# Optimization experiments

Hardware: AMD Instinct MI355X
Metric: run time of the kernel (lower is better)

Reference implementation:

```python
import jax, jax.numpy as jnp
import numpy as np

L, B, D = 1024, 4, 1024
E, K, H = 8, 2, 4096


def setup_inputs() -> dict:
    key = jax.random.key(0)
    ks = jax.random.split(key, 12)
    s_g = 1.0 / np.sqrt(D)
    s_h = 1.0 / np.sqrt(H)
    return {
        "inputs": jax.random.normal(ks[0], (L, B, D), jnp.float32),
        "task_param": jax.random.normal(ks[1], (B, D), jnp.float32),
        "gate_img_w": jax.random.normal(ks[2], (D, E), jnp.float32) * s_g,
        "gate_img_b": jnp.zeros((E,), jnp.float32),
        "gate_txt_w": jax.random.normal(ks[3], (D, E), jnp.float32) * s_g,
        "gate_txt_b": jnp.zeros((E,), jnp.float32),
        "task_gate_w": jax.random.normal(ks[4], (D, E), jnp.float32) * s_g,
        "task_gate_b": jnp.zeros((E,), jnp.float32),
        "alpha": jnp.float32(0.5),
        "w1": jax.random.normal(ks[5], (E, D, H), jnp.float32) * s_g,
        "w2": jax.random.normal(ks[6], (E, H, D), jnp.float32) * s_h,
        "is_text": 1,
    }


def reference(inputs, task_param, gate_img_w, gate_img_b, gate_txt_w, gate_txt_b,
              task_gate_w, task_gate_b, alpha, w1, w2, is_text):
    # task gate: (B, E) -> broadcast over L
    task_logits = (task_param @ task_gate_w + task_gate_b)[None]  # (1, B, E)
    if is_text:
        input_logits = inputs @ gate_txt_w + gate_txt_b  # (L, B, E)
    else:
        input_logits = inputs @ gate_img_w + gate_img_b
    gate_logits = (1.0 - alpha) * input_logits + alpha * task_logits  # (L, B, E)

    topk_vals, sel = jax.lax.top_k(gate_logits, K)  # (L, B, K)

    # auxiliary load-balancing loss
    soft = jax.nn.softmax(gate_logits.astype(jnp.float32), axis=-1)
    avg_weight = soft.mean(axis=(0, 1))                       # (E,)
    expert_mask = jax.nn.one_hot(sel, E).sum(axis=2)          # (L, B, E)
    avg_count = expert_mask.mean(axis=(0, 1))                 # (E,)
    l_aux = jnp.mean(avg_weight * avg_count) * E

    # renormalized top-k weights, combined per expert: (L, B, E)
    weights = jax.nn.softmax(topk_vals.astype(jnp.float32), axis=-1).astype(inputs.dtype)
    comb = jnp.sum(jax.nn.one_hot(sel, E, dtype=weights.dtype) * weights[..., None], axis=2)

    # dense per-expert FFN, weighted combine (loop over fixed small E)
    results = jnp.zeros_like(inputs)
    for e in range(E):
        h = jax.nn.gelu(inputs @ w1[e])      # (L, B, H)
        out = h @ w2[e]                      # (L, B, D)
        results = results + comb[..., e:e + 1] * out
    return results, l_aux.astype(jnp.float32)
```

## Files before the change

kernel.cpp:

```cpp
#include <hip/hip_runtime.h>
#include <hip/hip_bf16.h>
#include <math.h>

#define L_ 1024
#define B_ 4
#define D_ 1024
#define E_ 8
#define K_ 2
#define H_ 4096
#define T_ (L_*B_)
#define P_ (T_*K_)
#define PPAD (P_+256)

typedef unsigned short u16;
typedef __attribute__((ext_vector_type(4))) float f32x4;
typedef __attribute__((ext_vector_type(8))) short s16x8;

__device__ __forceinline__ u16 f2bf(float f) {
  uint32_t u = __float_as_uint(f);
  uint32_t r = (u + 0x7FFFu + ((u >> 16) & 1u)) >> 16;
  return (u16)r;
}
__device__ __forceinline__ float bf2f(u16 v) {
  return __uint_as_float((uint32_t)v << 16);
}
__device__ __forceinline__ float gelu_fast(float v) {
  float u = v * (1.0f + 0.044715f * v * v);
  float t = __expf(-1.5957691216057308f * u);
  return v / (1.0f + t);
}


__device__ void conv_block(const float* __restrict__ src, u16* __restrict__ dst,
                           int R, int C, int r0, int c0) {
  __shared__ float tile[64][65];
  int t = threadIdx.x;
  int tr = t >> 4, tc = (t & 15) * 4;
#pragma unroll
  for (int p = 0; p < 4; ++p) {
    int r = tr + p * 16;
    float4 v = *(const float4*)(src + (size_t)(r0 + r) * C + c0 + tc);
    tile[r][tc] = v.x; tile[r][tc+1] = v.y; tile[r][tc+2] = v.z; tile[r][tc+3] = v.w;
  }
  __syncthreads();
#pragma unroll
  for (int p = 0; p < 4; ++p) {
    int c = tr + p * 16;
    ushort4 o;
    o.x = f2bf(tile[tc+0][c]); o.y = f2bf(tile[tc+1][c]);
    o.z = f2bf(tile[tc+2][c]); o.w = f2bf(tile[tc+3][c]);
    *(ushort4*)(dst + (size_t)(c0 + c) * R + r0 + tc) = o;
  }
}

__global__ void prep(const float* __restrict__ w1, u16* __restrict__ w1b,
                     const float* __restrict__ x, const float* __restrict__ task_param,
                     const float* __restrict__ gw_img, const float* __restrict__ gb_img,
                     const float* __restrict__ gw_txt, const float* __restrict__ gb_txt,
                     const float* __restrict__ tgw, const float* __restrict__ tgb,
                     const float* __restrict__ alpha_p, const int* __restrict__ is_text_p,
                     float4* __restrict__ sel_w, float* __restrict__ prob_part,
                     int* __restrict__ count_part) {
  int gid = blockIdx.x;
  if (gid < 8192) {
    int gx = gid & 63, gy = (gid >> 6) & 15, e = gid >> 10;
    conv_block(w1 + (size_t)e * D_ * H_, w1b + (size_t)e * D_ * H_,
               D_, H_, gy * 64, gx * 64);
    return;
  }
  int bid = gid - 8192;
  __shared__ float wprob[4][8];
  __shared__ int wcnt[4][8];
  int wid = threadIdx.x >> 6, lane = threadIdx.x & 63;
  int t = bid * 4 + wid;
  int b = t & (B_ - 1);
  int it = is_text_p[0];
  const float* gw = it ? gw_txt : gw_img;
  const float* gb = it ? gb_txt : gb_img;
  float alpha = alpha_p[0];
  const float* xr = x + (size_t)t * D_;
  const float* tp = task_param + (size_t)b * D_;
  float acc[8] = {0,0,0,0,0,0,0,0};
  float tac[8] = {0,0,0,0,0,0,0,0};
  for (int i = 0; i < D_/64; ++i) {
    int d = i * 64 + lane;
    float xv = xr[d], tv = tp[d];
#pragma unroll
    for (int e = 0; e < 8; ++e) {
      acc[e] += xv * gw[d*8 + e];
      tac[e] += tv * tgw[d*8 + e];
    }
  }
#pragma unroll
  for (int e = 0; e < 8; ++e) {
#pragma unroll
    for (int off = 32; off > 0; off >>= 1) {
      acc[e] += __shfl_xor(acc[e], off);
      tac[e] += __shfl_xor(tac[e], off);
    }
  }
  float lg[8];
#pragma unroll
  for (int e = 0; e < 8; ++e)
    lg[e] = (1.0f - alpha) * (acc[e] + gb[e]) + alpha * (tac[e] + tgb[e]);
  float m = lg[0];
#pragma unroll
  for (int e = 1; e < 8; ++e) m = fmaxf(m, lg[e]);
  float pr[8], ps = 0.f;
#pragma unroll
  for (int e = 0; e < 8; ++e) { pr[e] = expf(lg[e] - m); ps += pr[e]; }
  float inv = 1.0f / ps;
  int i0 = 0; float v0 = lg[0];
#pragma unroll
  for (int e = 1; e < 8; ++e) if (lg[e] > v0) { v0 = lg[e]; i0 = e; }
  int i1 = -1; float v1 = -1e30f;
#pragma unroll
  for (int e = 0; e < 8; ++e) if (e != i0 && lg[e] > v1) { v1 = lg[e]; i1 = e; }
  float ex = expf(v1 - v0);
  float w0 = 1.0f / (1.0f + ex), w1v = ex / (1.0f + ex);
  if (lane == 0) {
    sel_w[t] = make_float4(__int_as_float(i0), __int_as_float(i1), w0, w1v);
#pragma unroll
    for (int e = 0; e < 8; ++e) {
      wprob[wid][e] = pr[e] * inv;
      wcnt[wid][e] = (i0 == e) + (i1 == e);
    }
  }
  __syncthreads();
  if (threadIdx.x < 8) {
    int e = threadIdx.x;
    prob_part[bid * 8 + e] = wprob[0][e] + wprob[1][e] + wprob[2][e] + wprob[3][e];
    count_part[bid * 8 + e] = wcnt[0][e] + wcnt[1][e] + wcnt[2][e] + wcnt[3][e];
  }
}

__global__ void finalize(const float* __restrict__ prob_part, const int* __restrict__ count_part,
                         int* __restrict__ meta, float* __restrict__ laux_out) {
  __shared__ float ps_[256];
  __shared__ int cs_[256];
  int t = threadIdx.x;
  int e = t & 7, s = t >> 3;
  float p = 0.f; int c = 0;
  for (int b = s; b < 1024; b += 32) { p += prob_part[b*8 + e]; c += count_part[b*8 + e]; }
  ps_[t] = p; cs_[t] = c;
  __syncthreads();
  for (int st = 16; st > 0; st >>= 1) {
    if (s < st) { ps_[t] += ps_[t + st*8]; cs_[t] += cs_[t + st*8]; }
    __syncthreads();
  }
  if (t == 0) {
    int off = 0; float laux = 0.f;
    int u1 = 0, u2 = 0;
    for (int ee = 0; ee < 8; ++ee) {
      int cnt = cs_[ee];
      meta[ee] = cnt;
      meta[8 + ee] = off;
      meta[16 + ee] = off;
      int nb = (cnt + 255) >> 8;
      meta[24 + ee] = nb;
      meta[32 + ee] = u1;
      meta[41 + ee] = u2;
      u1 += 16 * nb;
      u2 += 16 * nb;
      off += cnt;
      laux += (ps_[ee] * (1.0f/4096.0f)) * ((float)cnt * (1.0f/4096.0f));
    }
    meta[32 + 8] = u1;
    meta[41 + 8] = u2;
    meta[50] = 0;
    meta[51] = 0;
    *laux_out = laux;
  }
}

__global__ void scatter_gather(const float* __restrict__ x, const float4* __restrict__ sel_w,
                               int* __restrict__ cursors, float* __restrict__ pair_w,
                               int* __restrict__ pair_idx, u16* __restrict__ Xg) {
  int wid = threadIdx.x >> 6, lane = threadIdx.x & 63;
  int t = blockIdx.x * 4 + wid;
  float4 sw = sel_w[t];
  int s0 = __float_as_int(sw.x), s1 = __float_as_int(sw.y);
  int p0 = 0, p1 = 0;
  if (lane == 0) {
    p0 = atomicAdd(&cursors[s0], 1);
    p1 = atomicAdd(&cursors[s1], 1);
  }
  p0 = __shfl(p0, 0); p1 = __shfl(p1, 0);
  if (lane == 0) {
    pair_w[p0] = sw.z; pair_w[p1] = sw.w;
    pair_idx[t*2] = p0; pair_idx[t*2+1] = p1;
  }
  const float* xr = x + (size_t)t * D_;
  u16* d0 = Xg + (size_t)p0 * D_;
  u16* d1 = Xg + (size_t)p1 * D_;
#pragma unroll
  for (int i = 0; i < 4; ++i) {
    int c = i * 256 + lane * 4;
    float4 v = *(const float4*)(xr + c);
    ushort4 o;
    o.x = f2bf(v.x); o.y = f2bf(v.y); o.z = f2bf(v.z); o.w = f2bf(v.w);
    *(ushort4*)(d0 + c) = o;
    *(ushort4*)(d1 + c) = o;
  }
}

template<int EPI, int KDIM, int KLEN, int NOUT, int NPANEL, int KSPLIT, bool DOCONV>
__global__ __launch_bounds__(512, 2)
void gemm256(const u16* __restrict__ Tok, const u16* __restrict__ Wt,
             int* __restrict__ meta, const float* __restrict__ pair_w,
             u16* __restrict__ Hout, u16* __restrict__ Cout,
             const float* __restrict__ w2f, u16* __restrict__ w2b) {
  const int* offs = meta + 8;
  const int* nbx  = meta + 24;
  const int* ub   = (EPI == 0) ? meta + 32 : meta + 41;
  int* tick       = meta + ((EPI == 0) ? 50 : 51);

  __shared__ u16 As[2][16384];
  __shared__ u16 Bs[2][16384];
  __shared__ int s_u;
  int t = threadIdx.x, lane = t & 63, wid = t >> 6;
  int wf = wid & 1, wt = wid >> 1;

  int goff[4]; int ldso[4];
#pragma unroll
  for (int i = 0; i < 4; ++i) {
    int slot = i * 512 + t;
    int row = slot >> 3;
    int kk = (slot & 7) ^ (row & 7);
    goff[i] = row * KDIM + kk * 8;
    ldso[i] = slot * 8;
  }

  int aoff[8][2], boff[4][2];
#pragma unroll
  for (int r = 0; r < 8; ++r) {
    int row = wf * 128 + r * 16 + (lane & 15);
#pragma unroll
    for (int h = 0; h < 2; ++h) {
      int kk = h * 4 + (lane >> 4);
      aoff[r][h] = (row * 8 + (kk ^ (row & 7))) * 8;
    }
  }
#pragma unroll
  for (int f = 0; f < 4; ++f) {
    int row = wt * 64 + f * 16 + (lane & 15);
#pragma unroll
    for (int h = 0; h < 2; ++h) {
      int kk = h * 4 + (lane >> 4);
      boff[f][h] = (row * 8 + (kk ^ (row & 7))) * 8;
    }
  }

  constexpr int NT = KLEN / 64;
  int lr = lane & 15, lg4 = (lane >> 4) * 4;
  int Ugemm = ub[8];
  int Utot = DOCONV ? (Ugemm + 4096) : Ugemm;

  for (;;) {
    if (t == 0) s_u = atomicAdd(tick, 1);
    __syncthreads();
    int u = s_u;
    if (u >= Utot) break;

    if (DOCONV && u >= Ugemm) {
      int cu = u - Ugemm;
      int e = cu >> 9;
      int loc = cu & 511;
      int rb = loc >> 4, cb = loc & 15;
      int r0 = rb * 128, c0 = cb * 64;
      const float* src = w2f + (size_t)e * H_ * D_;
      u16* dst = w2b + (size_t)e * H_ * D_;
      float* tile = (float*)&As[0][0];
#pragma unroll
      for (int p = 0; p < 4; ++p) {
        int idx = p * 512 + t;
        int r = idx >> 4;
        int cq = (idx & 15) * 4;
        float4 v = *(const float4*)(src + (size_t)(r0 + r) * D_ + c0 + cq);
        float* tr = tile + r * 67 + cq;
        tr[0] = v.x; tr[1] = v.y; tr[2] = v.z; tr[3] = v.w;
      }
      __syncthreads();
      int c = t >> 3, rq0 = (t & 7) * 16;
#pragma unroll
      for (int j = 0; j < 16; j += 4) {
        ushort4 o;
        o.x = f2bf(tile[(rq0 + j + 0) * 67 + c]);
        o.y = f2bf(tile[(rq0 + j + 1) * 67 + c]);
        o.z = f2bf(tile[(rq0 + j + 2) * 67 + c]);
        o.w = f2bf(tile[(rq0 + j + 3) * 67 + c]);
        *(ushort4*)(dst + (size_t)(c0 + c) * H_ + r0 + rq0 + j) = o;
      }
      continue;
    }

    int e = 0;
    while (u >= ub[e + 1]) ++e;
    int ul = u - ub[e];
    int nb = nbx[e];
    int panel = ul / (nb * KSPLIT);
    int rem   = ul - panel * (nb * KSPLIT);
    int bx    = rem / KSPLIT;
    int ks    = rem - bx * KSPLIT;
    int ne  = meta[e];
    int off = offs[e];
    int kbase = ks * KLEN;
    u16* Cpart = Cout + (size_t)ks * P_ * D_;
    const u16* Wg = Wt + (size_t)e * NOUT * KDIM + (size_t)panel * 256 * KDIM + kbase;
    const u16* Tg = Tok + (size_t)(off + bx * 256) * KDIM + kbase;

    f32x4 acc[8][4] = {};
#pragma unroll
    for (int i = 0; i < 4; ++i) {
      __builtin_amdgcn_global_load_lds(
          (const __attribute__((address_space(1))) void*)(Wg + goff[i]),
          (__attribute__((address_space(3))) void*)(&As[0][ldso[i]]), 16, 0, 0);
      __builtin_amdgcn_global_load_lds(
          (const __attribute__((address_space(1))) void*)(Tg + goff[i]),
          (__attribute__((address_space(3))) void*)(&Bs[0][ldso[i]]), 16, 0, 0);
    }
    __syncthreads();
    int cur = 0;
    for (int tt = 0; tt < NT; ++tt) {
      if (tt + 1 < NT) {
        int k0 = (tt + 1) * 64;
        int nbuf = cur ^ 1;
#pragma unroll
        for (int i = 0; i < 4; ++i) {
          __builtin_amdgcn_global_load_lds(
              (const __attribute__((address_space(1))) void*)(Wg + goff[i] + k0),
              (__attribute__((address_space(3))) void*)(&As[nbuf][ldso[i]]), 16, 0, 0);
          __builtin_amdgcn_global_load_lds(
              (const __attribute__((address_space(1))) void*)(Tg + goff[i] + k0),
              (__attribute__((address_space(3))) void*)(&Bs[nbuf][ldso[i]]), 16, 0, 0);
        }
      }
      const u16* Ab = &As[cur][0]; const u16* Bb = &Bs[cur][0];
#pragma unroll
      for (int h = 0; h < 2; ++h) {
        s16x8 a[8], b[4];
#pragma unroll
        for (int r = 0; r < 8; ++r) a[r] = *(const s16x8*)(Ab + aoff[r][h]);
#pragma unroll
        for (int f = 0; f < 4; ++f) b[f] = *(const s16x8*)(Bb + boff[f][h]);
#pragma unroll
        for (int r = 0; r < 8; ++r)
#pragma unroll
          for (int f = 0; f < 4; ++f)
            acc[r][f] = __builtin_amdgcn_mfma_f32_16x16x32_bf16(a[r], b[f], acc[r][f], 0, 0, 0);
      }
      __syncthreads();
      cur ^= 1;
    }

#pragma unroll
    for (int f = 0; f < 4; ++f) {
      int tokl = bx * 256 + wt * 64 + f * 16 + lr;
      if (tokl >= ne) continue;
      size_t grow = (size_t)(off + tokl);
      if (EPI == 0) {
#pragma unroll
        for (int r = 0; r < 8; ++r) {
          ushort4 o;
          o.x = f2bf(gelu_fast(acc[r][f][0]));
          o.y = f2bf(gelu_fast(acc[r][f][1]));
          o.z = f2bf(gelu_fast(acc[r][f][2]));
          o.w = f2bf(gelu_fast(acc[r][f][3]));
          *(ushort4*)(Hout + grow * NOUT + panel * 256 + wf * 128 + r * 16 + lg4) = o;
        }
      } else {
        float w = pair_w[grow];
#pragma unroll
        for (int r = 0; r < 8; ++r) {
          ushort4 o;
          o.x = f2bf(acc[r][f][0] * w); o.y = f2bf(acc[r][f][1] * w);
          o.z = f2bf(acc[r][f][2] * w); o.w = f2bf(acc[r][f][3] * w);
          *(ushort4*)(Cpart + grow * NOUT + panel * 256 + wf * 128 + r * 16 + lg4) = o;
        }
      }
    }
  }
}

__global__ void combine(const u16* __restrict__ pair_out, const int* __restrict__ pair_idx,
                        float* __restrict__ out) {
  int t = blockIdx.x;
  int p0 = pair_idx[t*2], p1 = pair_idx[t*2+1];
  int c = threadIdx.x * 4;
  float ox = 0.f, oy = 0.f, oz = 0.f, ow = 0.f;
#pragma unroll
  for (int part = 0; part < 4; ++part) {
    const u16* pp = pair_out + (size_t)part * P_ * D_;
    ushort4 a = *(const ushort4*)(pp + (size_t)p0 * D_ + c);
    ushort4 b = *(const ushort4*)(pp + (size_t)p1 * D_ + c);
    ox += bf2f(a.x) + bf2f(b.x);
    oy += bf2f(a.y) + bf2f(b.y);
    oz += bf2f(a.z) + bf2f(b.z);
    ow += bf2f(a.w) + bf2f(b.w);
  }
  float4 o; o.x = ox; o.y = oy; o.z = oz; o.w = ow;
  *(float4*)(out + (size_t)t * D_ + c) = o;
}

extern "C" void kernel_launch(void* const* d_in, const int* in_sizes, int n_in,
                              void* d_out, int out_size, void* d_ws, size_t ws_size,
                              hipStream_t stream) {
  const float* inputs      = (const float*)d_in[0];
  const float* task_param  = (const float*)d_in[1];
  const float* gate_img_w  = (const float*)d_in[2];
  const float* gate_img_b  = (const float*)d_in[3];
  const float* gate_txt_w  = (const float*)d_in[4];
  const float* gate_txt_b  = (const float*)d_in[5];
  const float* task_gate_w = (const float*)d_in[6];
  const float* task_gate_b = (const float*)d_in[7];
  const float* alpha       = (const float*)d_in[8];
  const float* w1          = (const float*)d_in[9];
  const float* w2          = (const float*)d_in[10];
  const int*   is_text     = (const int*)d_in[11];
  float* out = (float*)d_out;

  char* ws = (char*)d_ws;
  u16* w1b = (u16*)(ws + 0);
  u16* w2b = (u16*)(ws + 67108864);
  u16* Xg  = (u16*)(ws + 134217728);
  u16* Hb  = (u16*)(ws + 151519232);
  float4* sel_w   = (float4*)(ws + 220725248);
  float* pair_w   = (float*)(ws + 220725248 + 65536);
  int* pair_idx   = (int*)(ws + 220725248 + 98816);
  float* prob_part= (float*)(ws + 220725248 + 131584);
  int* count_part = (int*)(ws + 220725248 + 164352);
  int* meta       = (int*)(ws + 220725248 + 197120);
  u16* pair_out   = (u16*)(ws + 0);

  prep<<<dim3(9216), 256, 0, stream>>>(w1, w1b,
      inputs, task_param, gate_img_w, gate_img_b, gate_txt_w, gate_txt_b,
      task_gate_w, task_gate_b, alpha, is_text, sel_w, prob_part, count_part);
  finalize<<<dim3(1), 256, 0, stream>>>(prob_part, count_part, meta,
      out + (size_t)T_ * D_);
  scatter_gather<<<dim3(T_/4), 256, 0, stream>>>(inputs, sel_w, meta + 16, pair_w, pair_idx, Xg);
  gemm256<0, D_, D_, H_, 16, 1, true><<<dim3(256), 512, 0, stream>>>(
      Xg, w1b, meta, pair_w, Hb, (u16*)nullptr, w2, w2b);
  gemm256<1, H_, H_/4, D_, 4, 4, false><<<dim3(256), 512, 0, stream>>>(
      Hb, w2b, meta, pair_w, (u16*)nullptr, pair_out, (const float*)nullptr, (u16*)nullptr);
  combine<<<dim3(T_), 256, 0, stream>>>(pair_out, pair_idx, out);
}
```

Baseline: 450.2 us.

## Shrink persistent grouped GEMM tiles to 128x128 with K=32 steps and more blocks

Rewrites the persistent grouped expert GEMM from 256x256 tiles with 512 threads and K-step 64 to 128x128 tiles with 256 threads, K-step 32 and a single 32KB shared buffer. The launch grows to 768 persistent blocks, and the in-GEMM w2 conversion now uses smaller 64x64 tiles through a shared helper. The aim is better occupancy and less tail and padding waste on small per-expert token counts. The cost is lower data reuse per tile, more tiles to schedule and twice as many barrier-separated K iterations.

```diff
diff --git a/kernel.cpp b/kernel.cpp
--- a/kernel.cpp
+++ b/kernel.cpp
@@ -31,24 +31,24 @@
 }
 
 
-__device__ void conv_block(const float* __restrict__ src, u16* __restrict__ dst,
-                           int R, int C, int r0, int c0) {
-  __shared__ float tile[64][65];
+__device__ void conv_tile(const float* __restrict__ src, u16* __restrict__ dst,
+                          int R, int C, int r0, int c0, float* tile ) {
   int t = threadIdx.x;
   int tr = t >> 4, tc = (t & 15) * 4;
 #pragma unroll
   for (int p = 0; p < 4; ++p) {
     int r = tr + p * 16;
     float4 v = *(const float4*)(src + (size_t)(r0 + r) * C + c0 + tc);
-    tile[r][tc] = v.x; tile[r][tc+1] = v.y; tile[r][tc+2] = v.z; tile[r][tc+3] = v.w;
+    float* tp = tile + r * 65 + tc;
+    tp[0] = v.x; tp[1] = v.y; tp[2] = v.z; tp[3] = v.w;
   }
   __syncthreads();
 #pragma unroll
   for (int p = 0; p < 4; ++p) {
     int c = tr + p * 16;
     ushort4 o;
-    o.x = f2bf(tile[tc+0][c]); o.y = f2bf(tile[tc+1][c]);
-    o.z = f2bf(tile[tc+2][c]); o.w = f2bf(tile[tc+3][c]);
+    o.x = f2bf(tile[(tc+0)*65 + c]); o.y = f2bf(tile[(tc+1)*65 + c]);
+    o.z = f2bf(tile[(tc+2)*65 + c]); o.w = f2bf(tile[(tc+3)*65 + c]);
     *(ushort4*)(dst + (size_t)(c0 + c) * R + r0 + tc) = o;
   }
 }
@@ -61,11 +61,12 @@
                      const float* __restrict__ alpha_p, const int* __restrict__ is_text_p,
                      float4* __restrict__ sel_w, float* __restrict__ prob_part,
                      int* __restrict__ count_part) {
+  __shared__ float tile[64*65];
   int gid = blockIdx.x;
   if (gid < 8192) {
     int gx = gid & 63, gy = (gid >> 6) & 15, e = gid >> 10;
-    conv_block(w1 + (size_t)e * D_ * H_, w1b + (size_t)e * D_ * H_,
-               D_, H_, gy * 64, gx * 64);
+    conv_tile(w1 + (size_t)e * D_ * H_, w1b + (size_t)e * D_ * H_,
+              D_, H_, gy * 64, gx * 64, tile);
     return;
   }
   int bid = gid - 8192;
@@ -156,12 +157,12 @@
       meta[ee] = cnt;
       meta[8 + ee] = off;
       meta[16 + ee] = off;
-      int nb = (cnt + 255) >> 8;
+      int nb = (cnt + 127) >> 7;
       meta[24 + ee] = nb;
       meta[32 + ee] = u1;
       meta[41 + ee] = u2;
-      u1 += 16 * nb;
-      u2 += 16 * nb;
+      u1 += 32 * nb;
+      u2 += 32 * nb;
       off += cnt;
       laux += (ps_[ee] * (1.0f/4096.0f)) * ((float)cnt * (1.0f/4096.0f));
     }
@@ -205,8 +206,8 @@
 }
 
 template<int EPI, int KDIM, int KLEN, int NOUT, int NPANEL, int KSPLIT, bool DOCONV>
-__global__ __launch_bounds__(512, 2)
-void gemm256(const u16* __restrict__ Tok, const u16* __restrict__ Wt,
+__global__ __launch_bounds__(256)
+void gemm128(const u16* __restrict__ Tok, const u16* __restrict__ Wt,
              int* __restrict__ meta, const float* __restrict__ pair_w,
              u16* __restrict__ Hout, u16* __restrict__ Cout,
              const float* __restrict__ w2f, u16* __restrict__ w2b) {
@@ -215,46 +216,35 @@
   const int* ub   = (EPI == 0) ? meta + 32 : meta + 41;
   int* tick       = meta + ((EPI == 0) ? 50 : 51);
 
-  __shared__ u16 As[2][16384];
-  __shared__ u16 Bs[2][16384];
+  __shared__ u16 lds[16384];
   __shared__ int s_u;
   int t = threadIdx.x, lane = t & 63, wid = t >> 6;
-  int wf = wid & 1, wt = wid >> 1;
-
-  int goff[4]; int ldso[4];
-#pragma unroll
-  for (int i = 0; i < 4; ++i) {
-    int slot = i * 512 + t;
-    int row = slot >> 3;
-    int kk = (slot & 7) ^ (row & 7);
+  int wm = (wid >> 1) * 64, wn = (wid & 1) * 64;
+
+  int goff[2], ldso[2];
+#pragma unroll
+  for (int i = 0; i < 2; ++i) {
+    int slot = i * 256 + t;
+    int row = slot >> 2;
+    int p = slot & 3;
+    int kk = p ^ ((row >> 1) & 3);
     goff[i] = row * KDIM + kk * 8;
     ldso[i] = slot * 8;
   }
 
-  int aoff[8][2], boff[4][2];
-#pragma unroll
-  for (int r = 0; r < 8; ++r) {
-    int row = wf * 128 + r * 16 + (lane & 15);
-#pragma unroll
-    for (int h = 0; h < 2; ++h) {
-      int kk = h * 4 + (lane >> 4);
-      aoff[r][h] = (row * 8 + (kk ^ (row & 7))) * 8;
-    }
-  }
-#pragma unroll
-  for (int f = 0; f < 4; ++f) {
-    int row = wt * 64 + f * 16 + (lane & 15);
-#pragma unroll
-    for (int h = 0; h < 2; ++h) {
-      int kk = h * 4 + (lane >> 4);
-      boff[f][h] = (row * 8 + (kk ^ (row & 7))) * 8;
-    }
-  }
-
-  constexpr int NT = KLEN / 64;
+  int aoff[4], boff[4];
+#pragma unroll
+  for (int r = 0; r < 4; ++r) {
+    int rowm = wm + r * 16 + (lane & 15);
+    aoff[r] = (rowm * 4 + ((lane >> 4) ^ ((rowm >> 1) & 3))) * 8;
+    int rown = wn + r * 16 + (lane & 15);
+    boff[r] = (rown * 4 + ((lane >> 4) ^ ((rown >> 1) & 3))) * 8;
+  }
+
+  constexpr int NT = KLEN / 32;
   int lr = lane & 15, lg4 = (lane >> 4) * 4;
   int Ugemm = ub[8];
-  int Utot = DOCONV ? (Ugemm + 4096) : Ugemm;
+  int Utot = DOCONV ? (Ugemm + 8192) : Ugemm;
 
   for (;;) {
     if (t == 0) s_u = atomicAdd(tick, 1);
@@ -264,33 +254,11 @@
 
     if (DOCONV && u >= Ugemm) {
       int cu = u - Ugemm;
-      int e = cu >> 9;
-      int loc = cu & 511;
+      int e = cu >> 10;
+      int loc = cu & 1023;
       int rb = loc >> 4, cb = loc & 15;
-      int r0 = rb * 128, c0 = cb * 64;
-      const float* src = w2f + (size_t)e * H_ * D_;
-      u16* dst = w2b + (size_t)e * H_ * D_;
-      float* tile = (float*)&As[0][0];
-#pragma unroll
-      for (int p = 0; p < 4; ++p) {
-        int idx = p * 512 + t;
-        int r = idx >> 4;
-        int cq = (idx & 15) * 4;
-        float4 v = *(const float4*)(src + (size_t)(r0 + r) * D_ + c0 + cq);
-        float* tr = tile + r * 67 + cq;
-        tr[0] = v.x; tr[1] = v.y; tr[2] = v.z; tr[3] = v.w;
-      }
-      __syncthreads();
-      int c = t >> 3, rq0 = (t & 7) * 16;
-#pragma unroll
-      for (int j = 0; j < 16; j += 4) {
-        ushort4 o;
-        o.x = f2bf(tile[(rq0 + j + 0) * 67 + c]);
-        o.y = f2bf(tile[(rq0 + j + 1) * 67 + c]);
-        o.z = f2bf(tile[(rq0 + j + 2) * 67 + c]);
-        o.w = f2bf(tile[(rq0 + j + 3) * 67 + c]);
-        *(ushort4*)(dst + (size_t)(c0 + c) * H_ + r0 + rq0 + j) = o;
-      }
+      conv_tile(w2f + (size_t)e * H_ * D_, w2b + (size_t)e * H_ * D_,
+                H_, D_, rb * 64, cb * 64, (float*)lds);
       continue;
     }
 
@@ -298,84 +266,88 @@
     while (u >= ub[e + 1]) ++e;
     int ul = u - ub[e];
     int nb = nbx[e];
-    int panel = ul / (nb * KSPLIT);
-    int rem   = ul - panel * (nb * KSPLIT);
-    int bx    = rem / KSPLIT;
-    int ks    = rem - bx * KSPLIT;
+    int panel, bx, ks;
+    if (EPI == 0) { panel = ul / nb; bx = ul - panel * nb; ks = 0; }
+    else {
+      panel = ul / (nb * KSPLIT);
+      int rem = ul - panel * (nb * KSPLIT);
+      bx = rem / KSPLIT;
+      ks = rem - bx * KSPLIT;
+    }
     int ne  = meta[e];
     int off = offs[e];
     int kbase = ks * KLEN;
     u16* Cpart = Cout + (size_t)ks * P_ * D_;
-    const u16* Wg = Wt + (size_t)e * NOUT * KDIM + (size_t)panel * 256 * KDIM + kbase;
-    const u16* Tg = Tok + (size_t)(off + bx * 256) * KDIM + kbase;
-
-    f32x4 acc[8][4] = {};
-#pragma unroll
-    for (int i = 0; i < 4; ++i) {
+    const u16* Wg = Wt + (size_t)e * NOUT * KDIM + (size_t)panel * 128 * KDIM + kbase;
+    const u16* Tg = Tok + (size_t)(off + bx * 128) * KDIM + kbase;
+    u16* As0 = lds; u16* Bs0 = lds + 8192;
+
+    f32x4 acc[4][4] = {};
+#pragma unroll
+    for (int i = 0; i < 2; ++i) {
       __builtin_amdgcn_global_load_lds(
           (const __attribute__((address_space(1))) void*)(Wg + goff[i]),
-          (__attribute__((address_space(3))) void*)(&As[0][ldso[i]]), 16, 0, 0);
+          (__attribute__((address_space(3))) void*)(As0 + ldso[i]), 16, 0, 0);
       __builtin_amdgcn_global_load_lds(
           (const __attribute__((address_space(1))) void*)(Tg + goff[i]),
-          (__attribute__((address_space(3))) void*)(&Bs[0][ldso[i]]), 16, 0, 0);
+          (__attribute__((address_space(3))) void*)(Bs0 + ldso[i]), 16, 0, 0);
     }
     __syncthreads();
     int cur = 0;
     for (int tt = 0; tt < NT; ++tt) {
       if (tt + 1 < NT) {
-        int k0 = (tt + 1) * 64;
+        int k0 = (tt + 1) * 32;
         int nbuf = cur ^ 1;
 #pragma unroll
-        for (int i = 0; i < 4; ++i) {
+        for (int i = 0; i < 2; ++i) {
           __builtin_amdgcn_global_load_lds(
               (const __attribute__((address_space(1))) void*)(Wg + goff[i] + k0),
-              (__attribute__((address_space(3))) void*)(&As[nbuf][ldso[i]]), 16, 0, 0);
+              (__attribute__((address_space(3))) void*)(As0 + nbuf * 4096 + ldso[i]), 16, 0, 0);
           __builtin_amdgcn_global_load_lds(
               (const __attribute__((address_space(1))) void*)(Tg + goff[i] + k0),
-              (__attribute__((address_space(3))) void*)(&Bs[nbuf][ldso[i]]), 16, 0, 0);
+              (__attribute__((address_space(3))) void*)(Bs0 + nbuf * 4096 + ldso[i]), 16, 0, 0);
         }
       }
-      const u16* Ab = &As[cur][0]; const u16* Bb = &Bs[cur][0];
-#pragma unroll
-      for (int h = 0; h < 2; ++h) {
-        s16x8 a[8], b[4];
-#pragma unroll
-        for (int r = 0; r < 8; ++r) a[r] = *(const s16x8*)(Ab + aoff[r][h]);
-#pragma unroll
-        for (int f = 0; f < 4; ++f) b[f] = *(const s16x8*)(Bb + boff[f][h]);
-#pragma unroll
-        for (int r = 0; r < 8; ++r)
-#pragma unroll
-          for (int f = 0; f < 4; ++f)
-            acc[r][f] = __builtin_amdgcn_mfma_f32_16x16x32_bf16(a[r], b[f], acc[r][f], 0, 0, 0);
+      const u16* Ab = As0 + cur * 4096;
+      const u16* Bb = Bs0 + cur * 4096;
+      s16x8 a[4], b[4];
+#pragma unroll
+      for (int r = 0; r < 4; ++r) {
+        a[r] = *(const s16x8*)(Ab + aoff[r]);
+        b[r] = *(const s16x8*)(Bb + boff[r]);
       }
+#pragma unroll
+      for (int r = 0; r < 4; ++r)
+#pragma unroll
+        for (int f = 0; f < 4; ++f)
+          acc[r][f] = __builtin_amdgcn_mfma_f32_16x16x32_bf16(a[r], b[f], acc[r][f], 0, 0, 0);
       __syncthreads();
       cur ^= 1;
     }
 
 #pragma unroll
     for (int f = 0; f < 4; ++f) {
-      int tokl = bx * 256 + wt * 64 + f * 16 + lr;
+      int tokl = bx * 128 + wn + f * 16 + lr;
       if (tokl >= ne) continue;
       size_t grow = (size_t)(off + tokl);
       if (EPI == 0) {
 #pragma unroll
-        for (int r = 0; r < 8; ++r) {
+        for (int r = 0; r < 4; ++r) {
           ushort4 o;
           o.x = f2bf(gelu_fast(acc[r][f][0]));
           o.y = f2bf(gelu_fast(acc[r][f][1]));
           o.z = f2bf(gelu_fast(acc[r][f][2]));
           o.w = f2bf(gelu_fast(acc[r][f][3]));
-          *(ushort4*)(Hout + grow * NOUT + panel * 256 + wf * 128 + r * 16 + lg4) = o;
+          *(ushort4*)(Hout + grow * NOUT + panel * 128 + wm + r * 16 + lg4) = o;
         }
       } else {
         float w = pair_w[grow];
 #pragma unroll
-        for (int r = 0; r < 8; ++r) {
+        for (int r = 0; r < 4; ++r) {
           ushort4 o;
           o.x = f2bf(acc[r][f][0] * w); o.y = f2bf(acc[r][f][1] * w);
           o.z = f2bf(acc[r][f][2] * w); o.w = f2bf(acc[r][f][3] * w);
-          *(ushort4*)(Cpart + grow * NOUT + panel * 256 + wf * 128 + r * 16 + lg4) = o;
+          *(ushort4*)(Cpart + grow * NOUT + panel * 128 + wm + r * 16 + lg4) = o;
         }
       }
     }
@@ -438,9 +410,9 @@
   finalize<<<dim3(1), 256, 0, stream>>>(prob_part, count_part, meta,
       out + (size_t)T_ * D_);
   scatter_gather<<<dim3(T_/4), 256, 0, stream>>>(inputs, sel_w, meta + 16, pair_w, pair_idx, Xg);
-  gemm256<0, D_, D_, H_, 16, 1, true><<<dim3(256), 512, 0, stream>>>(
+  gemm128<0, D_, D_, H_, 32, 1, true><<<dim3(768), 256, 0, stream>>>(
       Xg, w1b, meta, pair_w, Hb, (u16*)nullptr, w2, w2b);
-  gemm256<1, H_, H_/4, D_, 4, 4, false><<<dim3(256), 512, 0, stream>>>(
+  gemm128<1, H_, H_/4, D_, 8, 4, false><<<dim3(768), 256, 0, stream>>>(
       Hb, w2b, meta, pair_w, (u16*)nullptr, pair_out, (const float*)nullptr, (u16*)nullptr);
   combine<<<dim3(T_), 256, 0, stream>>>(pair_out, pair_idx, out);
 }
```

Result: slower. 824.9 us (+83.2%).

## Interleave global-to-LDS prefetch with MFMA phases using explicit waitcnt and barriers

Applied to the files above, without the earlier changes.

Replaces the simple double-buffered K loop of the grouped expert GEMM with a hand-scheduled pipeline. Each 64-wide K tile is split into four phases, and each phase issues a pair of async global-to-LDS loads for upcoming tiles alongside its MFMAs. Explicit vmcnt/lgkmcnt waits, s_barrier, sched_barrier and setprio control ordering. The goal is finer overlap of memory traffic with matrix math and fewer full-workgroup stalls. This relies on hand-tuned wait counts that must match the load issue order exactly. Redundant loads at the tail are clamped to the last tile.

```diff
diff --git a/kernel.cpp b/kernel.cpp
--- a/kernel.cpp
+++ b/kernel.cpp
@@ -252,9 +252,56 @@
   }
 
   constexpr int NT = KLEN / 64;
+  constexpr int NITER = NT / 2;
   int lr = lane & 15, lg4 = (lane >> 4) * 4;
   int Ugemm = ub[8];
   int Utot = DOCONV ? (Ugemm + 4096) : Ugemm;
+
+#define STA(b, q, tk) __builtin_amdgcn_global_load_lds( \
+      (const __attribute__((address_space(1))) void*)(Wg + goff[q] + (tk) * 64), \
+      (__attribute__((address_space(3))) void*)(&As[b][ldso[q]]), 16, 0, 0)
+#define STB(b, q, tk) __builtin_amdgcn_global_load_lds( \
+      (const __attribute__((address_space(1))) void*)(Tg + goff[q] + (tk) * 64), \
+      (__attribute__((address_space(3))) void*)(&Bs[b][ldso[q]]), 16, 0, 0)
+
+#define PH(MP, TB, DOB, VM, LG8, ...)                                          \
+  {                                                                            \
+    s16x8 a00 = *(const s16x8*)(&As[TB][aoff[(MP)*2+0][0]]);                   \
+    s16x8 a01 = *(const s16x8*)(&As[TB][aoff[(MP)*2+0][1]]);                   \
+    s16x8 a10 = *(const s16x8*)(&As[TB][aoff[(MP)*2+1][0]]);                   \
+    s16x8 a11 = *(const s16x8*)(&As[TB][aoff[(MP)*2+1][1]]);                   \
+    if (DOB) {                                                                 \
+      _Pragma("unroll")                                                        \
+      for (int nf = 0; nf < 4; ++nf) {                                         \
+        bn[nf][0] = *(const s16x8*)(&Bs[TB][boff[nf][0]]);                     \
+        bn[nf][1] = *(const s16x8*)(&Bs[TB][boff[nf][1]]);                     \
+      }                                                                        \
+    }                                                                          \
+    __VA_ARGS__;                                                               \
+    if (LG8) asm volatile("s_waitcnt lgkmcnt(8)" ::: "memory");                \
+    __builtin_amdgcn_s_barrier();                                              \
+    asm volatile("s_waitcnt lgkmcnt(0)" ::: "memory");                         \
+    __builtin_amdgcn_sched_barrier(0);                                         \
+    __builtin_amdgcn_s_setprio(1);                                             \
+    _Pragma("unroll")                                                          \
+    for (int nf = 0; nf < 4; ++nf) {                                           \
+      acc[(MP)*2+0][nf] = __builtin_amdgcn_mfma_f32_16x16x32_bf16(             \
+          a00, bn[nf][0], acc[(MP)*2+0][nf], 0, 0, 0);                         \
+      acc[(MP)*2+1][nf] = __builtin_amdgcn_mfma_f32_16x16x32_bf16(             \
+          a10, bn[nf][0], acc[(MP)*2+1][nf], 0, 0, 0);                         \
+    }                                                                          \
+    _Pragma("unroll")                                                          \
+    for (int nf = 0; nf < 4; ++nf) {                                           \
+      acc[(MP)*2+0][nf] = __builtin_amdgcn_mfma_f32_16x16x32_bf16(             \
+          a01, bn[nf][1], acc[(MP)*2+0][nf], 0, 0, 0);                         \
+      acc[(MP)*2+1][nf] = __builtin_amdgcn_mfma_f32_16x16x32_bf16(             \
+          a11, bn[nf][1], acc[(MP)*2+1][nf], 0, 0, 0);                         \
+    }                                                                          \
+    __builtin_amdgcn_s_setprio(0);                                             \
+    if (VM == 8)  asm volatile("s_waitcnt vmcnt(8)"  ::: "memory");            \
+    if (VM == 10) asm volatile("s_waitcnt vmcnt(10)" ::: "memory");            \
+    __builtin_amdgcn_s_barrier();                                              \
+  }
 
   for (;;) {
     if (t == 0) s_u = atomicAdd(tick, 1);
@@ -310,47 +357,30 @@
     const u16* Tg = Tok + (size_t)(off + bx * 256) * KDIM + kbase;
 
     f32x4 acc[8][4] = {};
-#pragma unroll
-    for (int i = 0; i < 4; ++i) {
-      __builtin_amdgcn_global_load_lds(
-          (const __attribute__((address_space(1))) void*)(Wg + goff[i]),
-          (__attribute__((address_space(3))) void*)(&As[0][ldso[i]]), 16, 0, 0);
-      __builtin_amdgcn_global_load_lds(
-          (const __attribute__((address_space(1))) void*)(Tg + goff[i]),
-          (__attribute__((address_space(3))) void*)(&Bs[0][ldso[i]]), 16, 0, 0);
-    }
-    __syncthreads();
-    int cur = 0;
-    for (int tt = 0; tt < NT; ++tt) {
-      if (tt + 1 < NT) {
-        int k0 = (tt + 1) * 64;
-        int nbuf = cur ^ 1;
-#pragma unroll
-        for (int i = 0; i < 4; ++i) {
-          __builtin_amdgcn_global_load_lds(
-              (const __attribute__((address_space(1))) void*)(Wg + goff[i] + k0),
-              (__attribute__((address_space(3))) void*)(&As[nbuf][ldso[i]]), 16, 0, 0);
-          __builtin_amdgcn_global_load_lds(
-              (const __attribute__((address_space(1))) void*)(Tg + goff[i] + k0),
-              (__attribute__((address_space(3))) void*)(&Bs[nbuf][ldso[i]]), 16, 0, 0);
-        }
-      }
-      const u16* Ab = &As[cur][0]; const u16* Bb = &Bs[cur][0];
-#pragma unroll
-      for (int h = 0; h < 2; ++h) {
-        s16x8 a[8], b[4];
-#pragma unroll
-        for (int r = 0; r < 8; ++r) a[r] = *(const s16x8*)(Ab + aoff[r][h]);
-#pragma unroll
-        for (int f = 0; f < 4; ++f) b[f] = *(const s16x8*)(Bb + boff[f][h]);
-#pragma unroll
-        for (int r = 0; r < 8; ++r)
-#pragma unroll
-          for (int f = 0; f < 4; ++f)
-            acc[r][f] = __builtin_amdgcn_mfma_f32_16x16x32_bf16(a[r], b[f], acc[r][f], 0, 0, 0);
-      }
-      __syncthreads();
-      cur ^= 1;
+    s16x8 bn[4][2];
+
+    STB(0, 0, 0); STB(0, 1, 0);
+    STB(0, 2, 0); STB(0, 3, 0);
+    STA(0, 0, 0); STA(0, 2, 0);
+    STA(0, 1, 0); STA(0, 3, 0);
+    STB(1, 0, 1); STB(1, 1, 1);
+    STB(1, 2, 1); STB(1, 3, 1);
+    STA(1, 0, 1); STA(1, 2, 1);
+    asm volatile("s_waitcnt vmcnt(8)" ::: "memory");
+    __builtin_amdgcn_s_barrier();
+
+    for (int j = 0; j < NITER; ++j) {
+      int t1 = 2 * j + 1;
+      int tc2 = (2 * j + 2 < NT) ? 2 * j + 2 : NT - 1;
+      int tc3 = (2 * j + 3 < NT) ? 2 * j + 3 : NT - 1;
+      PH(0, 0, 1,  0, 1, STA(1, 1, t1); STA(1, 3, t1));
+      PH(1, 0, 0, 10, 0, STB(0, 0, tc2); STB(0, 1, tc2));
+      PH(2, 0, 0,  0, 0, STB(0, 2, tc2); STB(0, 3, tc2));
+      PH(3, 0, 0,  8, 0, STA(0, 0, tc2); STA(0, 2, tc2));
+      PH(0, 1, 1,  0, 1, STA(0, 1, tc2); STA(0, 3, tc2));
+      PH(1, 1, 0, 10, 0, STB(1, 0, tc3); STB(1, 1, tc3));
+      PH(2, 1, 0,  0, 0, STB(1, 2, tc3); STB(1, 3, tc3));
+      PH(3, 1, 0,  8, 0, STA(1, 0, tc3); STA(1, 2, tc3));
     }
 
 #pragma unroll
@@ -380,6 +410,9 @@
       }
     }
   }
+#undef PH
+#undef STA
+#undef STB
 }
 
 __global__ void combine(const u16* __restrict__ pair_out, const int* __restrict__ pair_idx,
```

New measurement: 459.9 us. +2.2%, slower.
